# Optimization experiments

Hardware: AMD Instinct MI355X
Metric: run time of the kernel (lower is better)

The kernel has to match this reference:

```python
import jax, jax.numpy as jnp
import numpy as np

B, T, S, D, V, L = 32, 128, 256, 1024, 10000, 2
EOS = 2


def setup_inputs() -> dict:
    key = jax.random.key(0)
    ks = jax.random.split(key, 12)
    s = 0.02
    targets = jax.random.randint(ks[0], (B, T), 0, V)
    targets = jnp.where(targets == EOS, 3, targets)  # decoder strips eos; keep rectangular
    return {
        'encoder_outputs': jax.random.normal(ks[1], (B, S, D), jnp.float32),
        'targets': targets,
        'emb': jax.random.normal(ks[2], (V, D)) * s,
        'W_ih': jax.random.normal(ks[3], (L, 4 * D, D)) * s,
        'W_hh': jax.random.normal(ks[4], (L, 4 * D, D)) * s,
        'b_ih': jnp.zeros((L, 4 * D)),
        'b_hh': jnp.zeros((L, 4 * D)),
        'Wconv': jax.random.normal(ks[5], (D, 3)) * s,   # Conv1d(1 -> attn_dim, k=3) kernel
        'bconv': jnp.zeros((D,)),
        'Wq': jax.random.normal(ks[6], (D, D)) * s,      # query_proj (no bias)
        'Wv': jax.random.normal(ks[7], (D, D)) * s,      # value_proj (no bias)
        'attn_bias': jax.random.uniform(ks[8], (D,), minval=-0.1, maxval=0.1),
        'fc_attn_w': jax.random.normal(ks[9], (D,)) * s, # attention score fc (D -> 1)
        'fc_attn_b': jnp.zeros(()),
        'fc1_w': jax.random.normal(ks[10], (D, 2 * D)) * s,  # Linear(2D -> D)
        'fc1_b': jnp.zeros((D,)),
        'fc2_w': jax.random.normal(ks[11], (V, D)) * s,      # Linear(D -> V)
        'fc2_b': jnp.zeros((V,)),
    }


def _forward(encoder_outputs, targets, emb, W_ih, W_hh, b_ih, b_hh, Wconv, bconv,
             Wq, Wv, attn_bias, fc_attn_w, fc_attn_b, fc1_w, fc1_b, fc2_w, fc2_b):
    b, s_len = encoder_outputs.shape[0], encoder_outputs.shape[1]
    # value_proj(encoder_outputs) is constant across decode steps
    vproj = jnp.einsum('bsd,ed->bse', encoder_outputs, Wv)
    embedded = emb[targets]                  # (B,T,D)
    xs = jnp.swapaxes(embedded, 0, 1)        # (T,B,D)
    h0 = jnp.zeros((L, b, D), embedded.dtype)
    c0 = jnp.zeros((L, b, D), embedded.dtype)
    a0 = jnp.zeros((b, s_len), embedded.dtype)  # last alignment energy starts at zero

    def step(carry, x_t):
        h, c, attn = carry
        inp = x_t
        hs, cs = [], []
        for l in range(L):  # fixed small number of LSTM layers
            gates = inp @ W_ih[l].T + b_ih[l] + h[l] @ W_hh[l].T + b_hh[l]
            i, f, g, o = jnp.split(gates, 4, axis=-1)
            c_l = jax.nn.sigmoid(f) * c[l] + jax.nn.sigmoid(i) * jnp.tanh(g)
            h_l = jax.nn.sigmoid(o) * jnp.tanh(c_l)
            hs.append(h_l); cs.append(c_l); inp = h_l
        q = inp  # decoder rnn output for this step, (B,D)
        # location_conv: Conv1d(1->D, k=3, pad=1) over last alignment
        pad = jnp.pad(attn, ((0, 0), (1, 1)))
        win = jnp.stack([pad[:, :-2], pad[:, 1:-1], pad[:, 2:]], axis=-1)  # (B,S,3)
        loc = jnp.einsum('bsk,dk->bsd', win, Wconv) + bconv
        qp = q @ Wq.T
        e = jnp.tanh(qp[:, None, :] + vproj + loc + attn_bias)  # (B,S,D)
        energy = jnp.einsum('bsd,d->bs', e, fc_attn_w) + fc_attn_b
        new_attn = jax.nn.softmax(energy, axis=-1)
        context = jnp.einsum('bs,bsd->bd', new_attn, encoder_outputs)
        hid = jnp.tanh(jnp.concatenate([q, context], axis=-1) @ fc1_w.T + fc1_b)
        logp = jax.nn.log_softmax(hid @ fc2_w.T + fc2_b, axis=-1)
        return (jnp.stack(hs), jnp.stack(cs), new_attn), logp

    _, logps = jax.lax.scan(step, (h0, c0, a0), xs)  # (T,B,V)
    return jnp.swapaxes(logps, 0, 1)                 # (B,T,V) log-probs


def reference(encoder_outputs, targets, emb, W_ih, W_hh, b_ih, b_hh, Wconv, bconv,
              Wq, Wv, attn_bias, fc_attn_w, fc_attn_b, fc1_w, fc1_b, fc2_w, fc2_b):
    return _forward(encoder_outputs, targets, emb, W_ih, W_hh, b_ih, b_hh, Wconv, bconv,
                    Wq, Wv, attn_bias, fc_attn_w, fc_attn_b, fc1_w, fc1_b, fc2_w, fc2_b)
```

## Files before the change

### kernel.cpp

```cpp
#include <hip/hip_runtime.h>
#include <stdint.h>

#define B_ 32
#define T_ 128
#define S_ 256
#define D_ 1024
#define V_ 10000

typedef unsigned short u16;
typedef unsigned long long u64;
typedef __attribute__((ext_vector_type(8))) short bf16x8;
typedef __attribute__((ext_vector_type(4))) float f32x4;

__device__ __forceinline__ float bf2f(u16 u){ union { unsigned int i; float f; } v; v.i = ((unsigned int)u)<<16; return v.f; }
__device__ __forceinline__ u16 f2bf(float f){ union { float ff; unsigned int i; } v; v.ff = f; unsigned int x = v.i; return (u16)((x + 0x7fffu + ((x>>16)&1u))>>16); }
__device__ __forceinline__ float ftanh(float x){
  float e = __expf(2.f*x);
  return __builtin_fmaf(-2.f, __builtin_amdgcn_rcpf(1.f+e), 1.f);
}
__device__ __forceinline__ float sigm(float x){
  return __builtin_amdgcn_rcpf(1.f + __expf(-x));
}

__global__ void k_cast(const float* __restrict__ in, u16* __restrict__ out, long n){
  for (long i = (long)blockIdx.x*blockDim.x + threadIdx.x; i < n; i += (long)gridDim.x*blockDim.x)
    out[i] = f2bf(in[i]);
}

__global__ void k_w1cat(const float* __restrict__ wih1, const float* __restrict__ whh1, u16* __restrict__ out){
  const long n = (long)4096*2048;
  for (long i = (long)blockIdx.x*blockDim.x + threadIdx.x; i < n; i += (long)gridDim.x*blockDim.x){
    int row = (int)(i >> 11), k = (int)(i & 2047);
    float v = (k < D_) ? wih1[(size_t)row*D_ + k] : whh1[(size_t)row*D_ + (k - D_)];
    out[i] = f2bf(v);
  }
}

__global__ void k_bias(const float* __restrict__ bih, const float* __restrict__ bhh,
                       const float* __restrict__ bcv, const float* __restrict__ abias,
                       const float* __restrict__ Wcv, const float* __restrict__ fcw,
                       float* __restrict__ bias0, float* __restrict__ bias1,
                       float* __restrict__ biasE, float* __restrict__ convw){
  int i = blockIdx.x*blockDim.x + threadIdx.x;
  if (i < 4096){ bias0[i] = bih[i]+bhh[i]; bias1[i] = bih[4096+i]+bhh[4096+i]; }
  if (i < 1024){
    biasE[i] = bcv[i]+abias[i];
    convw[i*4+0]=Wcv[i*3+0]; convw[i*4+1]=Wcv[i*3+1]; convw[i*4+2]=Wcv[i*3+2]; convw[i*4+3]=fcw[i];
  }
}

__global__ void k_gather(const float* __restrict__ emb, const int* __restrict__ tgt, u16* __restrict__ embA){
  int row = blockIdx.x;
  int t = row >> 5, b = row & 31;
  int e = tgt[b*T_ + t];
  const float* src = emb + (size_t)e*D_;
  u16* dst = embA + (size_t)row*D_;
  for (int d = threadIdx.x; d < D_; d += 256) dst[d] = f2bf(src[d]);
}

__device__ __forceinline__ void gld_lds(const u16* g, u16* l){
  __builtin_amdgcn_global_load_lds((const __attribute__((address_space(1))) unsigned int*)g,
                                   (__attribute__((address_space(3))) unsigned int*)l, 16, 0, 0);
}

template<int OUT_MODE, bool SWIZ>
__global__ __launch_bounds__(256) void k_gemm128(const u16* __restrict__ Am, const u16* __restrict__ Bm,
      const float* __restrict__ bias, void* __restrict__ Cout, int M, int N, int K, int lda, int ldc)
{
  __shared__ u16 As[128*32];
  __shared__ u16 Bs[128*32];
  int bm = blockIdx.y*128, bn = blockIdx.x*128;
  int tid = threadIdx.x;
  int wv = tid>>6, lane = tid&63;
  int wm = (wv>>1)*64, wn = (wv&1)*64;
  int r = lane&15, kh = lane>>4;
  f32x4 zero = {0.f,0.f,0.f,0.f};
  f32x4 acc[4][4];
  #pragma unroll
  for (int mi=0;mi<4;mi++)
    #pragma unroll
    for (int ni=0;ni<4;ni++) acc[mi][ni] = zero;

  for (int k0 = 0; k0 < K; k0 += 32){
    #pragma unroll
    for (int i=0;i<2;i++){
      int c = tid + i*256;
      int row = c>>2, ko = (c&3)*8;
      int ga = bm+row; if (ga > M-1) ga = M-1;
      gld_lds(Am + (size_t)ga*lda + k0 + ko, As + c*8);
      int gb = bn+row; if (gb > N-1) gb = N-1;
      gld_lds(Bm + (size_t)gb*K + k0 + ko, Bs + c*8);
    }
    __syncthreads();
    bf16x8 af[4], bfv[4];
    #pragma unroll
    for (int mi=0;mi<4;mi++) af[mi]  = *(const bf16x8*)(As + (wm+mi*16+r)*32 + kh*8);
    #pragma unroll
    for (int ni=0;ni<4;ni++) bfv[ni] = *(const bf16x8*)(Bs + (wn+ni*16+r)*32 + kh*8);
    #pragma unroll
    for (int mi=0;mi<4;mi++)
      #pragma unroll
      for (int ni=0;ni<4;ni++)
        acc[mi][ni] = __builtin_amdgcn_mfma_f32_16x16x32_bf16(af[mi], bfv[ni], acc[mi][ni], 0,0,0);
    __syncthreads();
  }
  #pragma unroll
  for (int mi=0;mi<4;mi++)
    #pragma unroll
    for (int ni=0;ni<4;ni++)
      #pragma unroll
      for (int rr=0;rr<4;rr++){
        int grow = bm+wm+mi*16+kh*4+rr;
        int gcol = bn+wn+ni*16+r;
        if (grow < M && gcol < N){
          float v = acc[mi][ni][rr];
          if (bias) v += bias[gcol];
          size_t orow = SWIZ ? (size_t)((grow&31)*T_ + (grow>>5)) : (size_t)grow;
          if (OUT_MODE==0)      ((float*)Cout)[orow*(size_t)ldc + gcol] = v;
          else if (OUT_MODE==1) ((u16*)Cout)[orow*(size_t)ldc + gcol] = f2bf(v);
          else                  ((u16*)Cout)[orow*(size_t)ldc + gcol] = f2bf(ftanh(v));
        }
      }
}

__device__ __forceinline__ void xcd_barrier(int* barL, int it){
  asm volatile("s_waitcnt vmcnt(0)" ::: "memory");
  __syncthreads();
  if (threadIdx.x==0){
    int grp = blockIdx.x & 7;
    int* gcnt = barL + grp*32;
    int* root = barL + 256;
    int* rel  = barL + 320 + grp*32;
    int v = __hip_atomic_fetch_add(gcnt, 1, __ATOMIC_RELAXED, __HIP_MEMORY_SCOPE_AGENT);
    if (v == 32*(it+1) - 1){
      int rv = __hip_atomic_fetch_add(root, 1, __ATOMIC_RELAXED, __HIP_MEMORY_SCOPE_AGENT);
      if (rv == 8*(it+1) - 1){
        #pragma unroll
        for (int g2=0; g2<8; ++g2)
          __hip_atomic_store(barL + 320 + g2*32, it+1, __ATOMIC_RELAXED, __HIP_MEMORY_SCOPE_AGENT);
      }
    }
    while (__hip_atomic_load(rel, __ATOMIC_RELAXED, __HIP_MEMORY_SCOPE_AGENT) < it+1)
      __builtin_amdgcn_s_sleep(4);
  }
  __syncthreads();
}

__device__ __forceinline__ void ring_barrier(int* cnt, int nblk, int it){
  asm volatile("s_waitcnt vmcnt(0)" ::: "memory");
  __syncthreads();
  if (threadIdx.x==0){
    __hip_atomic_fetch_add(cnt, 1, __ATOMIC_RELAXED, __HIP_MEMORY_SCOPE_AGENT);
    int target = nblk*(it+1);
    while (__hip_atomic_load(cnt, __ATOMIC_RELAXED, __HIP_MEMORY_SCOPE_AGENT) < target)
      __builtin_amdgcn_s_sleep(4);
  }
  __syncthreads();
}

__global__ __launch_bounds__(512) void k_lstm_p(const u16* __restrict__ Whh0, const u16* __restrict__ W1cat,
    const u16* __restrict__ Wqm, const u16* __restrict__ X0, const float* __restrict__ bias1,
    u16* __restrict__ Hh, u16* __restrict__ qcat, u16* __restrict__ qps, int* __restrict__ barL)
{
  __shared__ u16 W0s[16*1024];
  __shared__ u16 W1s[16*2048];
  __shared__ u16 Wqs[4*1024];
  __shared__ float gl0[8*544];
  __shared__ float gl1[8*544];
  __shared__ float glq[4*128];
  __shared__ u16 hb0[128];
  __shared__ u16 hb1[128];
  int bid = blockIdx.x, tid = threadIdx.x;
  int w = tid>>6, lane = tid&63, r = lane&15, kh = lane>>4;
  for (int ci = tid; ci < 2048; ci += 512){
    int row = ci>>7, c = ci&127;
    int grow = (row>>2)*1024 + bid*4 + (row&3);
    bf16x8 v = *(const bf16x8*)(Whh0 + (size_t)grow*1024 + c*8);
    *(bf16x8*)(W0s + (size_t)(((row<<7) + (c ^ (row&7)))*8)) = v;
  }
  for (int ci = tid; ci < 4096; ci += 512){
    int row = ci>>8, c = ci&255;
    int grow = (row>>2)*1024 + bid*4 + (row&3);
    bf16x8 v = *(const bf16x8*)(W1cat + (size_t)grow*2048 + c*8);
    *(bf16x8*)(W1s + (size_t)(((row<<8) + (c ^ (row&7)))*8)) = v;
  }
  {
    int row = tid>>7, c = tid&127;
    bf16x8 v = *(const bf16x8*)(Wqm + (size_t)(bid*4+row)*1024 + c*8);
    *(bf16x8*)(Wqs + (size_t)(((row<<7) + (c ^ (row&7)))*8)) = v;
  }
  __syncthreads();
  float c0reg = 0.f, c1reg = 0.f;
  int cb = tid>>2, cj = tid&3;
  int col = bid*4 + cj;
  float b1i=0.f, b1f=0.f, b1g=0.f, b1o=0.f;
  if (tid < 128){ b1i=bias1[col]; b1f=bias1[1024+col]; b1g=bias1[2048+col]; b1o=bias1[3072+col]; }
  for (int p = 0; p <= T_+1; ++p){
    const u16* Hprev = Hh + (size_t)p*65536;
    u16* Hcur = (u16*)Hh + (size_t)(p+1)*65536;
    bool doG0 = (p < T_);
    bool doG1 = (p >= 1 && p <= T_);
    bool loadG1 = (p >= 1);
    bool doQP = (p >= 2);
    float x_gi=0.f, x_gf=0.f, x_gg=0.f, x_go=0.f;
    if (doG0 && tid < 128){
      const u16* xr = X0 + ((size_t)p*32 + cb)*4096 + col;
      x_gi = bf2f(xr[0]); x_gf = bf2f(xr[1024]); x_gg = bf2f(xr[2048]); x_go = bf2f(xr[3072]);
    }
    f32x4 acc00={0.f,0.f,0.f,0.f}, acc01={0.f,0.f,0.f,0.f};
    f32x4 acc10={0.f,0.f,0.f,0.f}, acc11={0.f,0.f,0.f,0.f};
    f32x4 accq0={0.f,0.f,0.f,0.f}, accq1={0.f,0.f,0.f,0.f};
    bf16x8 a_g0[2][4], a_g1[2][8];
    if (doG0){
      const u16* a0 = Hprev + (size_t)r*2048 + w*128 + kh*8;
      const u16* a1 = Hprev + (size_t)(16+r)*2048 + w*128 + kh*8;
      #pragma unroll
      for (int kk=0;kk<4;kk++){ a_g0[0][kk] = *(const bf16x8*)(a0 + kk*32);
                                a_g0[1][kk] = *(const bf16x8*)(a1 + kk*32); }
    }
    if (loadG1){
      const u16* a0 = Hprev + (size_t)r*2048 + w*256 + kh*8;
      const u16* a1 = Hprev + (size_t)(16+r)*2048 + w*256 + kh*8;
      #pragma unroll
      for (int kk=0;kk<8;kk++){ a_g1[0][kk] = *(const bf16x8*)(a0 + kk*32);
                                a_g1[1][kk] = *(const bf16x8*)(a1 + kk*32); }
    }
    if (doG0){
      #pragma unroll
      for (int kk=0;kk<4;kk++){
        int c = (w<<4) + (kk<<2) + kh;
        bf16x8 bv = *(const bf16x8*)(W0s + (size_t)((((int)r<<7) + (c ^ (r&7)))*8));
        acc00 = __builtin_amdgcn_mfma_f32_16x16x32_bf16(a_g0[0][kk], bv, acc00, 0,0,0);
        acc01 = __builtin_amdgcn_mfma_f32_16x16x32_bf16(a_g0[1][kk], bv, acc01, 0,0,0);
      }
    }
    if (doG1){
      #pragma unroll
      for (int kk=0;kk<8;kk++){
        int c = (w<<5) + (kk<<2) + kh;
        bf16x8 bv = *(const bf16x8*)(W1s + (size_t)((((int)r<<8) + (c ^ (r&7)))*8));
        acc10 = __builtin_amdgcn_mfma_f32_16x16x32_bf16(a_g1[0][kk], bv, acc10, 0,0,0);
        acc11 = __builtin_amdgcn_mfma_f32_16x16x32_bf16(a_g1[1][kk], bv, acc11, 0,0,0);
      }
    }
    if (doQP && w >= 4){
      #pragma unroll
      for (int kk=0;kk<8;kk++){
        int c = ((w-4)<<5) + (kk<<2) + kh;
        int qrw = r & 3;
        bf16x8 bv = *(const bf16x8*)(Wqs + (size_t)(((qrw<<7) + (c ^ (qrw&7)))*8));
        accq0 = __builtin_amdgcn_mfma_f32_16x16x32_bf16(a_g1[0][kk], bv, accq0, 0,0,0);
        accq1 = __builtin_amdgcn_mfma_f32_16x16x32_bf16(a_g1[1][kk], bv, accq1, 0,0,0);
      }
    }
    #pragma unroll
    for (int rr=0;rr<4;rr++){
      gl0[w*544 + (kh*4+rr)*17 + r]    = acc00[rr];
      gl0[w*544 + (16+kh*4+rr)*17 + r] = acc01[rr];
      gl1[w*544 + (kh*4+rr)*17 + r]    = acc10[rr];
      gl1[w*544 + (16+kh*4+rr)*17 + r] = acc11[rr];
    }
    if (doQP && w >= 4 && r < 4){
      #pragma unroll
      for (int rr=0;rr<4;rr++){
        glq[(w-4)*128 + (kh*4+rr)*4 + r]    = accq0[rr];
        glq[(w-4)*128 + (16+kh*4+rr)*4 + r] = accq1[rr];
      }
    }
    __syncthreads();
    if (tid < 128){
      if (doG0){
        float gi=x_gi, gf=x_gf, gg=x_gg, go=x_go;
        #pragma unroll
        for (int ww=0;ww<8;ww++){
          const float* gp = gl0 + ww*544 + cb*17 + cj;
          gi += gp[0]; gf += gp[4]; gg += gp[8]; go += gp[12];
        }
        float cn = sigm(gf)*c0reg + sigm(gi)*ftanh(gg);
        float hn = sigm(go)*ftanh(cn); c0reg = cn;
        hb0[tid] = f2bf(hn);
      }
      if (doG1){
        float gi=b1i, gf=b1f, gg=b1g, go=b1o;
        #pragma unroll
        for (int ww=0;ww<8;ww++){
          const float* gp = gl1 + ww*544 + cb*17 + cj;
          gi += gp[0]; gf += gp[4]; gg += gp[8]; go += gp[12];
        }
        float cn = sigm(gf)*c1reg + sigm(gi)*ftanh(gg);
        float hn = sigm(go)*ftanh(cn); c1reg = cn;
        hb1[tid] = f2bf(hn);
      }
      if (doQP){
        float hq = glq[cb*4+cj] + glq[128 + cb*4+cj] + glq[256 + cb*4+cj] + glq[384 + cb*4+cj];
        qps[((size_t)(p-2)*32 + cb)*1024 + col] = f2bf(hq);
      }
    }
    __syncthreads();
    if (tid < 32){
      union { u64 v; u16 s[4]; } pk;
      if (doG0){
        pk.s[0]=hb0[tid*4]; pk.s[1]=hb0[tid*4+1]; pk.s[2]=hb0[tid*4+2]; pk.s[3]=hb0[tid*4+3];
        __hip_atomic_store((u64*)(Hcur + (size_t)tid*2048 + bid*4), pk.v,
                           __ATOMIC_RELAXED, __HIP_MEMORY_SCOPE_AGENT);
      }
      if (doG1){
        pk.s[0]=hb1[tid*4]; pk.s[1]=hb1[tid*4+1]; pk.s[2]=hb1[tid*4+2]; pk.s[3]=hb1[tid*4+3];
        __hip_atomic_store((u64*)(Hcur + (size_t)tid*2048 + 1024 + bid*4), pk.v,
                           __ATOMIC_RELAXED, __HIP_MEMORY_SCOPE_AGENT);
        *(u64*)(qcat + ((size_t)(p-1)*32 + tid)*2048 + bid*4) = pk.v;
      }
    }
    if (p < T_+1) xcd_barrier(barL, p);
  }
}

__global__ __launch_bounds__(512) void k_attn_p(const u16* __restrict__ vpb, const u16* __restrict__ qpb,
    const u16* __restrict__ enc, const float* __restrict__ convw,
    float* __restrict__ eng, u16* __restrict__ qcat, int* __restrict__ barA)
{
  __shared__ float aw[256];
  __shared__ float cred[512];
  int bid = blockIdx.x, tid = threadIdx.x;
  int b = bid>>3, p = bid&7;
  int w = tid>>6, lane = tid&63;
  int d0 = lane*16;
  f32x4 cw[16];
  #pragma unroll
  for (int j=0;j<16;j++) cw[j] = *(const f32x4*)(convw + (size_t)(d0+j)*4);
  if (tid < 256) aw[tid] = 0.f;
  __syncthreads();
  int* cnt = barA + b*32;
  for (int t=0; t<T_; ++t){
    float* ebuf = eng + (t&1)*8192 + b*256;
    const u16* qrow = qpb + ((size_t)t*32 + b)*1024 + d0;
    bf16x8 q0 = *(const bf16x8*)qrow, q1 = *(const bf16x8*)(qrow+8);
    float qf[16];
    #pragma unroll
    for (int j=0;j<16;j++) qf[j] = bf2f((u16)(j<8 ? q0[j] : q1[j-8]));
    #pragma unroll
    for (int ss=0; ss<4; ++ss){
      int s = p*32 + w*4 + ss;
      float am = (s>0)   ? aw[s-1] : 0.f;
      float ac =           aw[s];
      float ap = (s<255) ? aw[s+1] : 0.f;
      const u16* vrow = vpb + ((size_t)(b*256+s))*1024 + d0;
      bf16x8 v0 = *(const bf16x8*)vrow, v1 = *(const bf16x8*)(vrow+8);
      float sum = 0.f;
      #pragma unroll
      for (int j=0;j<16;j++){
        float vv = bf2f((u16)(j<8 ? v0[j] : v1[j-8]));
        float x = qf[j] + vv + am*cw[j][0] + ac*cw[j][1] + ap*cw[j][2];
        sum += ftanh(x)*cw[j][3];
      }
      #pragma unroll
      for (int o=32;o;o>>=1) sum += __shfl_xor(sum, o);
      if (lane==0)
        __hip_atomic_store(ebuf + s, sum, __ATOMIC_RELAXED, __HIP_MEMORY_SCOPE_AGENT);
    }
    ring_barrier(cnt, 8, t);
    if (w == 0){
      float e0 = __hip_atomic_load(ebuf + lane*4+0, __ATOMIC_RELAXED, __HIP_MEMORY_SCOPE_AGENT);
      float e1 = __hip_atomic_load(ebuf + lane*4+1, __ATOMIC_RELAXED, __HIP_MEMORY_SCOPE_AGENT);
      float e2 = __hip_atomic_load(ebuf + lane*4+2, __ATOMIC_RELAXED, __HIP_MEMORY_SCOPE_AGENT);
      float e3 = __hip_atomic_load(ebuf + lane*4+3, __ATOMIC_RELAXED, __HIP_MEMORY_SCOPE_AGENT);
      float m = fmaxf(fmaxf(e0,e1), fmaxf(e2,e3));
      #pragma unroll
      for (int o=32;o;o>>=1) m = fmaxf(m, __shfl_xor(m,o));
      float x0 = __expf(e0-m), x1 = __expf(e1-m), x2 = __expf(e2-m), x3 = __expf(e3-m);
      float sl = x0+x1+x2+x3;
      #pragma unroll
      for (int o=32;o;o>>=1) sl += __shfl_xor(sl,o);
      float inv = __builtin_amdgcn_rcpf(sl);
      aw[lane*4+0] = x0*inv; aw[lane*4+1] = x1*inv;
      aw[lane*4+2] = x2*inv; aw[lane*4+3] = x3*inv;
    }
    __syncthreads();
    int sq = tid>>7, dt = tid&127;
    const u16* ep = enc + (size_t)(b*256 + sq*64)*1024 + p*128 + dt;
    float a0=0.f,a1=0.f,a2=0.f,a3=0.f;
    #pragma unroll 4
    for (int s2=0;s2<64;s2+=4){
      a0 += aw[sq*64+s2]   * bf2f(ep[(size_t)(s2)  *1024]);
      a1 += aw[sq*64+s2+1] * bf2f(ep[(size_t)(s2+1)*1024]);
      a2 += aw[sq*64+s2+2] * bf2f(ep[(size_t)(s2+2)*1024]);
      a3 += aw[sq*64+s2+3] * bf2f(ep[(size_t)(s2+3)*1024]);
    }
    cred[tid] = a0+a1+a2+a3;
    __syncthreads();
    if (tid < 128)
      qcat[((size_t)t*32 + b)*2048 + 1024 + p*128 + tid] =
        f2bf(cred[tid]+cred[128+tid]+cred[256+tid]+cred[384+tid]);
  }
}

__global__ __launch_bounds__(256) void k_logsm(float* __restrict__ out){
  int row = blockIdx.x, tid = threadIdx.x;
  float* p = out + (size_t)row*V_;
  __shared__ float red[4];
  float pv[40];
  int nv = 0;
  float mx = -3.0e38f;
  for (int v=tid; v<V_; v+=256){ float x = p[v]; pv[nv++] = x; mx = fmaxf(mx, x); }
  #pragma unroll
  for (int o=32;o;o>>=1) mx = fmaxf(mx, __shfl_xor(mx,o));
  if ((tid&63)==0) red[tid>>6]=mx;
  __syncthreads();
  mx = fmaxf(fmaxf(red[0],red[1]),fmaxf(red[2],red[3]));
  __syncthreads();
  float s = 0.f;
  for (int i=0;i<nv;i++) s += __expf(pv[i]-mx);
  #pragma unroll
  for (int o=32;o;o>>=1) s += __shfl_xor(s,o);
  if ((tid&63)==0) red[tid>>6]=s;
  __syncthreads();
  float lz = mx + __logf(red[0]+red[1]+red[2]+red[3]);
  { int i=0; for (int v=tid; v<V_; v+=256) p[v] = pv[i++] - lz; }
}

extern "C" void kernel_launch(void* const* d_in, const int* in_sizes, int n_in,
                              void* d_out, int out_size, void* d_ws, size_t ws_size,
                              hipStream_t stream)
{
  const float* enc   = (const float*)d_in[0];
  const int*   tgt   = (const int*)  d_in[1];
  const float* emb   = (const float*)d_in[2];
  const float* Wih   = (const float*)d_in[3];
  const float* Whh   = (const float*)d_in[4];
  const float* bih   = (const float*)d_in[5];
  const float* bhh   = (const float*)d_in[6];
  const float* Wcv   = (const float*)d_in[7];
  const float* bcv   = (const float*)d_in[8];
  const float* Wq    = (const float*)d_in[9];
  const float* Wvm   = (const float*)d_in[10];
  const float* abias = (const float*)d_in[11];
  const float* fcw   = (const float*)d_in[12];
  const float* fc1w  = (const float*)d_in[14];
  const float* fc1b  = (const float*)d_in[15];
  const float* fc2w  = (const float*)d_in[16];
  const float* fc2b  = (const float*)d_in[17];
  float* out = (float*)d_out;

  char* base = (char*)d_ws; size_t off = 0;
  auto A = [&](size_t nbytes)->char*{ char* q = base + off; off += (nbytes + 255) & ~(size_t)255; return q; };
  u16* enc_bf  = (u16*)A(8388608ull*2);
  u16* Wv_bf   = (u16*)A(1048576ull*2);
  u16* Wih0_bf = (u16*)A(4194304ull*2);
  u16* W1cat   = (u16*)A(8388608ull*2);
  u16* Whh0_bf = (u16*)A(4194304ull*2);
  u16* Wq_bf   = (u16*)A(1048576ull*2);
  u16* fc1w_bf = (u16*)A(2097152ull*2);
  u16* fc2w_bf = (u16*)A(10240000ull*2);
  u16* embA    = (u16*)A(4194304ull*2);
  u16* X0      = (u16*)A(16777216ull*2);
  u16* vpb     = (u16*)A(8388608ull*2);
  u16* qcat    = (u16*)A(8388608ull*2);
  float* bias0 = (float*)A(4096*4);
  float* bias1 = (float*)A(4096*4);
  float* biasE = (float*)A(1024*4);
  float* convw = (float*)A(4096*4);
  float* eng   = (float*)A(2*8192*4);
  int* barL    = (int*)A(4096);
  int* barA    = (int*)A(4096);
  u16* Hh      = fc2w_bf;
  u16* qps     = embA;
  u16* hid     = embA;

  hipMemsetAsync(Hh, 0, 2*65536*2, stream);
  hipMemsetAsync(barL, 0, 4096, stream);
  hipMemsetAsync(barA, 0, 4096, stream);

  k_cast<<<2048,256,0,stream>>>(enc,  enc_bf,  8388608);
  k_cast<<<1024,256,0,stream>>>(Wih,  Wih0_bf, 4194304);
  k_cast<<<1024,256,0,stream>>>(Whh,  Whh0_bf, 4194304);
  k_cast<<<512,256,0,stream>>>(Wq,    Wq_bf,   1048576);
  k_cast<<<512,256,0,stream>>>(Wvm,   Wv_bf,   1048576);
  k_cast<<<512,256,0,stream>>>(fc1w,  fc1w_bf, 2097152);
  k_w1cat<<<2048,256,0,stream>>>(Wih + 4194304, Whh + 4194304, W1cat);
  k_bias<<<16,256,0,stream>>>(bih, bhh, bcv, abias, Wcv, fcw, bias0, bias1, biasE, convw);
  k_gather<<<4096,256,0,stream>>>(emb, tgt, embA);

  k_gemm128<1,false><<<dim3(8,64),256,0,stream>>>(enc_bf, Wv_bf, biasE, vpb, 8192, 1024, 1024, 1024, 1024);
  k_gemm128<1,false><<<dim3(32,32),256,0,stream>>>(embA, Wih0_bf, bias0, X0, 4096, 4096, 1024, 1024, 4096);

  {
    const u16* a0 = Whh0_bf; const u16* a1 = W1cat; const u16* a2 = Wq_bf; const u16* a3 = X0;
    const float* a4 = bias1; u16* a5 = Hh; u16* a6 = qcat; u16* a7 = qps; int* a8 = barL;
    void* args[] = {(void*)&a0,(void*)&a1,(void*)&a2,(void*)&a3,(void*)&a4,(void*)&a5,
                    (void*)&a6,(void*)&a7,(void*)&a8};
    hipError_t e = hipLaunchCooperativeKernel((const void*)k_lstm_p, dim3(256), dim3(512), args, 0, stream);
    if (e != hipSuccess)
      k_lstm_p<<<dim3(256),dim3(512),0,stream>>>(a0,a1,a2,a3,a4,a5,a6,a7,a8);
  }

  {
    const u16* a0 = vpb; const u16* a1 = qps; const u16* a2 = enc_bf; const float* a3 = convw;
    float* a4 = eng; u16* a5 = qcat; int* a6 = barA;
    void* args[] = {(void*)&a0,(void*)&a1,(void*)&a2,(void*)&a3,(void*)&a4,(void*)&a5,(void*)&a6};
    hipError_t e = hipLaunchCooperativeKernel((const void*)k_attn_p, dim3(256), dim3(512), args, 0, stream);
    if (e != hipSuccess)
      k_attn_p<<<dim3(256),dim3(512),0,stream>>>(a0,a1,a2,a3,a4,a5,a6);
  }

  k_gemm128<2,false><<<dim3(8,32),256,0,stream>>>(qcat, fc1w_bf, fc1b, hid, 4096, 1024, 2048, 2048, 1024);
  k_cast<<<2048,256,0,stream>>>(fc2w, fc2w_bf, 10240000);
  k_gemm128<0,true><<<dim3(79,32),256,0,stream>>>(hid, fc2w_bf, fc2b, out, 4096, V_, 1024, 1024, V_);
  k_logsm<<<4096,256,0,stream>>>(out);
}
```

Baseline: 2.786 ms.

## Store value projection and encoder outputs as FP8 for attention loop

The value projection and a copy of the encoder outputs are now stored as 8-bit floats (custom e4m3-like encoding, clamped to ±240), so the per-step attention kernel reads half as many bytes when computing energies and context. The LSTM kernel also drops a shared-memory staging step and a block barrier, writing each hidden element directly with 16-bit atomic stores instead of packed 64-bit ones. The cost is lower precision in the attention energies and context, an extra cast kernel, and more scattered narrow global stores.

```diff
diff --git a/kernel.cpp b/kernel.cpp
--- a/kernel.cpp
+++ b/kernel.cpp
@@ -8,12 +8,27 @@
 #define V_ 10000
 
 typedef unsigned short u16;
+typedef unsigned char u8;
 typedef unsigned long long u64;
 typedef __attribute__((ext_vector_type(8))) short bf16x8;
 typedef __attribute__((ext_vector_type(4))) float f32x4;
+typedef __attribute__((ext_vector_type(4))) unsigned int u32x4;
 
 __device__ __forceinline__ float bf2f(u16 u){ union { unsigned int i; float f; } v; v.i = ((unsigned int)u)<<16; return v.f; }
 __device__ __forceinline__ u16 f2bf(float f){ union { float ff; unsigned int i; } v; v.ff = f; unsigned int x = v.i; return (u16)((x + 0x7fffu + ((x>>16)&1u))>>16); }
+__device__ __forceinline__ float fp82f(unsigned int x){
+  union { unsigned int i; float f; } v;
+  v.i = ((x & 0x80u) << 24) | ((x & 0x7Fu) << 20);
+  return v.f * 0x1.0p+120f;
+}
+__device__ __forceinline__ u8 f2fp8(float f){
+  union { float ff; unsigned int i; } v;
+  v.ff = fminf(fmaxf(f, -240.f), 240.f) * 0x1.0p-120f;
+  unsigned int s = (v.i >> 24) & 0x80u;
+  unsigned int u = v.i & 0x7FFFFFFFu;
+  u += ((u >> 20) & 1u) + 0x7FFFFu;
+  return (u8)(s | ((u >> 20) & 0x7Fu));
+}
 __device__ __forceinline__ float ftanh(float x){
   float e = __expf(2.f*x);
   return __builtin_fmaf(-2.f, __builtin_amdgcn_rcpf(1.f+e), 1.f);
@@ -25,6 +40,11 @@
 __global__ void k_cast(const float* __restrict__ in, u16* __restrict__ out, long n){
   for (long i = (long)blockIdx.x*blockDim.x + threadIdx.x; i < n; i += (long)gridDim.x*blockDim.x)
     out[i] = f2bf(in[i]);
+}
+
+__global__ void k_cast8(const float* __restrict__ in, u8* __restrict__ out, long n){
+  for (long i = (long)blockIdx.x*blockDim.x + threadIdx.x; i < n; i += (long)gridDim.x*blockDim.x)
+    out[i] = f2fp8(in[i]);
 }
 
 __global__ void k_w1cat(const float* __restrict__ wih1, const float* __restrict__ whh1, u16* __restrict__ out){
@@ -118,7 +138,8 @@
           size_t orow = SWIZ ? (size_t)((grow&31)*T_ + (grow>>5)) : (size_t)grow;
           if (OUT_MODE==0)      ((float*)Cout)[orow*(size_t)ldc + gcol] = v;
           else if (OUT_MODE==1) ((u16*)Cout)[orow*(size_t)ldc + gcol] = f2bf(v);
-          else                  ((u16*)Cout)[orow*(size_t)ldc + gcol] = f2bf(ftanh(v));
+          else if (OUT_MODE==2) ((u16*)Cout)[orow*(size_t)ldc + gcol] = f2bf(ftanh(v));
+          else                  ((u8*)Cout)[orow*(size_t)ldc + gcol] = f2fp8(v);
         }
       }
 }
@@ -168,8 +189,6 @@
   __shared__ float gl0[8*544];
   __shared__ float gl1[8*544];
   __shared__ float glq[4*128];
-  __shared__ u16 hb0[128];
-  __shared__ u16 hb1[128];
   int bid = blockIdx.x, tid = threadIdx.x;
   int w = tid>>6, lane = tid&63, r = lane&15, kh = lane>>4;
   for (int ci = tid; ci < 2048; ci += 512){
@@ -278,7 +297,8 @@
         }
         float cn = sigm(gf)*c0reg + sigm(gi)*ftanh(gg);
         float hn = sigm(go)*ftanh(cn); c0reg = cn;
-        hb0[tid] = f2bf(hn);
+        __hip_atomic_store(Hcur + (size_t)cb*2048 + col, f2bf(hn),
+                           __ATOMIC_RELAXED, __HIP_MEMORY_SCOPE_AGENT);
       }
       if (doG1){
         float gi=b1i, gf=b1f, gg=b1g, go=b1o;
@@ -289,34 +309,22 @@
         }
         float cn = sigm(gf)*c1reg + sigm(gi)*ftanh(gg);
         float hn = sigm(go)*ftanh(cn); c1reg = cn;
-        hb1[tid] = f2bf(hn);
+        u16 hb = f2bf(hn);
+        __hip_atomic_store(Hcur + (size_t)cb*2048 + 1024 + col, hb,
+                           __ATOMIC_RELAXED, __HIP_MEMORY_SCOPE_AGENT);
+        qcat[((size_t)(p-1)*32 + cb)*2048 + col] = hb;
       }
       if (doQP){
         float hq = glq[cb*4+cj] + glq[128 + cb*4+cj] + glq[256 + cb*4+cj] + glq[384 + cb*4+cj];
         qps[((size_t)(p-2)*32 + cb)*1024 + col] = f2bf(hq);
       }
     }
-    __syncthreads();
-    if (tid < 32){
-      union { u64 v; u16 s[4]; } pk;
-      if (doG0){
-        pk.s[0]=hb0[tid*4]; pk.s[1]=hb0[tid*4+1]; pk.s[2]=hb0[tid*4+2]; pk.s[3]=hb0[tid*4+3];
-        __hip_atomic_store((u64*)(Hcur + (size_t)tid*2048 + bid*4), pk.v,
-                           __ATOMIC_RELAXED, __HIP_MEMORY_SCOPE_AGENT);
-      }
-      if (doG1){
-        pk.s[0]=hb1[tid*4]; pk.s[1]=hb1[tid*4+1]; pk.s[2]=hb1[tid*4+2]; pk.s[3]=hb1[tid*4+3];
-        __hip_atomic_store((u64*)(Hcur + (size_t)tid*2048 + 1024 + bid*4), pk.v,
-                           __ATOMIC_RELAXED, __HIP_MEMORY_SCOPE_AGENT);
-        *(u64*)(qcat + ((size_t)(p-1)*32 + tid)*2048 + bid*4) = pk.v;
-      }
-    }
     if (p < T_+1) xcd_barrier(barL, p);
   }
 }
 
-__global__ __launch_bounds__(512) void k_attn_p(const u16* __restrict__ vpb, const u16* __restrict__ qpb,
-    const u16* __restrict__ enc, const float* __restrict__ convw,
+__global__ __launch_bounds__(512) void k_attn_p(const u8* __restrict__ vp8, const u16* __restrict__ qpb,
+    const u8* __restrict__ enc8, const float* __restrict__ convw,
     float* __restrict__ eng, u16* __restrict__ qcat, int* __restrict__ barA)
 {
   __shared__ float aw[256];
@@ -344,12 +352,12 @@
       float am = (s>0)   ? aw[s-1] : 0.f;
       float ac =           aw[s];
       float ap = (s<255) ? aw[s+1] : 0.f;
-      const u16* vrow = vpb + ((size_t)(b*256+s))*1024 + d0;
-      bf16x8 v0 = *(const bf16x8*)vrow, v1 = *(const bf16x8*)(vrow+8);
+      const u32x4 vv4 = *(const u32x4*)(vp8 + ((size_t)(b*256+s))*1024 + d0);
       float sum = 0.f;
       #pragma unroll
       for (int j=0;j<16;j++){
-        float vv = bf2f((u16)(j<8 ? v0[j] : v1[j-8]));
+        unsigned int word = vv4[j>>2];
+        float vv = fp82f((word >> ((j&3)*8)) & 0xFFu);
         float x = qf[j] + vv + am*cw[j][0] + ac*cw[j][1] + ap*cw[j][2];
         sum += ftanh(x)*cw[j][3];
       }
@@ -377,14 +385,14 @@
     }
     __syncthreads();
     int sq = tid>>7, dt = tid&127;
-    const u16* ep = enc + (size_t)(b*256 + sq*64)*1024 + p*128 + dt;
+    const u8* ep = enc8 + (size_t)(b*256 + sq*64)*1024 + p*128 + dt;
     float a0=0.f,a1=0.f,a2=0.f,a3=0.f;
     #pragma unroll 4
     for (int s2=0;s2<64;s2+=4){
-      a0 += aw[sq*64+s2]   * bf2f(ep[(size_t)(s2)  *1024]);
-      a1 += aw[sq*64+s2+1] * bf2f(ep[(size_t)(s2+1)*1024]);
-      a2 += aw[sq*64+s2+2] * bf2f(ep[(size_t)(s2+2)*1024]);
-      a3 += aw[sq*64+s2+3] * bf2f(ep[(size_t)(s2+3)*1024]);
+      a0 += aw[sq*64+s2]   * fp82f(ep[(size_t)(s2)  *1024]);
+      a1 += aw[sq*64+s2+1] * fp82f(ep[(size_t)(s2+1)*1024]);
+      a2 += aw[sq*64+s2+2] * fp82f(ep[(size_t)(s2+2)*1024]);
+      a3 += aw[sq*64+s2+3] * fp82f(ep[(size_t)(s2+3)*1024]);
     }
     cred[tid] = a0+a1+a2+a3;
     __syncthreads();
@@ -453,7 +461,8 @@
   u16* fc2w_bf = (u16*)A(10240000ull*2);
   u16* embA    = (u16*)A(4194304ull*2);
   u16* X0      = (u16*)A(16777216ull*2);
-  u16* vpb     = (u16*)A(8388608ull*2);
+  u8*  vp8     = (u8*)A(8388608ull);
+  u8*  enc8    = (u8*)A(8388608ull);
   u16* qcat    = (u16*)A(8388608ull*2);
   float* bias0 = (float*)A(4096*4);
   float* bias1 = (float*)A(4096*4);
@@ -471,6 +480,7 @@
   hipMemsetAsync(barA, 0, 4096, stream);
 
   k_cast<<<2048,256,0,stream>>>(enc,  enc_bf,  8388608);
+  k_cast8<<<2048,256,0,stream>>>(enc, enc8,    8388608);
   k_cast<<<1024,256,0,stream>>>(Wih,  Wih0_bf, 4194304);
   k_cast<<<1024,256,0,stream>>>(Whh,  Whh0_bf, 4194304);
   k_cast<<<512,256,0,stream>>>(Wq,    Wq_bf,   1048576);
@@ -480,7 +490,7 @@
   k_bias<<<16,256,0,stream>>>(bih, bhh, bcv, abias, Wcv, fcw, bias0, bias1, biasE, convw);
   k_gather<<<4096,256,0,stream>>>(emb, tgt, embA);
 
-  k_gemm128<1,false><<<dim3(8,64),256,0,stream>>>(enc_bf, Wv_bf, biasE, vpb, 8192, 1024, 1024, 1024, 1024);
+  k_gemm128<3,false><<<dim3(8,64),256,0,stream>>>(enc_bf, Wv_bf, biasE, vp8, 8192, 1024, 1024, 1024, 1024);
   k_gemm128<1,false><<<dim3(32,32),256,0,stream>>>(embA, Wih0_bf, bias0, X0, 4096, 4096, 1024, 1024, 4096);
 
   {
@@ -494,7 +504,7 @@
   }
 
   {
-    const u16* a0 = vpb; const u16* a1 = qps; const u16* a2 = enc_bf; const float* a3 = convw;
+    const u8* a0 = vp8; const u16* a1 = qps; const u8* a2 = enc8; const float* a3 = convw;
     float* a4 = eng; u16* a5 = qcat; int* a6 = barA;
     void* args[] = {(void*)&a0,(void*)&a1,(void*)&a2,(void*)&a3,(void*)&a4,(void*)&a5,(void*)&a6};
     hipError_t e = hipLaunchCooperativeKernel((const void*)k_attn_p, dim3(256), dim3(512), args, 0, stream);
```

After: 2.831 ms. Within noise of the previous version (+1.6%).
